# Kernel tuning notes

Measured on AMD Instinct MI355X. Metric: run time of the kernel, lower is better.

The kernel has to match this reference:

```python
import jax, jax.numpy as jnp
import numpy as np

NUM_CATEGORIES = 16
INPUT_DIM = 1024
HIDDEN_DIM = 4096
BATCH = 64
SEQ = 256


def setup_inputs() -> dict:
    key = jax.random.key(0)
    k1, k2, k3 = jax.random.split(key, 3)
    x = jax.random.normal(k1, (BATCH, SEQ, INPUT_DIM), dtype=jnp.float32)
    cat_ids = jax.random.randint(k2, (BATCH,), 0, NUM_CATEGORIES, dtype=jnp.int64)
    W = 0.02 * jax.random.normal(k3, (NUM_CATEGORIES, INPUT_DIM, HIDDEN_DIM), dtype=jnp.float32)
    b = jnp.zeros((NUM_CATEGORIES, HIDDEN_DIM), dtype=jnp.float32)
    return {"x": x, "cat_ids": cat_ids, "W": W, "b": b}


def reference(x, cat_ids, W, b):
    # Gather per-sample expert weights then batched matmul, matching torch.bmm semantics.
    selected_W = W[cat_ids]            # [B, input_dim, hidden_dim]
    selected_b = b[cat_ids]            # [B, hidden_dim]
    out = jnp.einsum('bsi,bih->bsh', x, selected_W) + selected_b[:, None, :]
    return out
```

## Files before the change

### kernel.cpp

```cpp
#include <hip/hip_runtime.h>
#include <hip/hip_bf16.h>
#include <stdint.h>

#define BATCH 64
#define SEQ   256
#define KDIM  1024
#define NDIM  4096
#define NCAT  16

#define BM 128
#define BN 128
#define BK 64
#define MT (SEQ/BM)
#define NT (NDIM/BN)
#define TILES_PER_BATCH (MT*NT)
#define NBLOCKS (BATCH*TILES_PER_BATCH)

typedef __attribute__((ext_vector_type(4))) float f32x4;
typedef __attribute__((ext_vector_type(4))) unsigned int u32x4;
typedef __attribute__((ext_vector_type(8))) short bf16x8;

__device__ __forceinline__ unsigned short f2bf(float f) {
  __hip_bfloat16 h = __float2bfloat16(f);
  return __builtin_bit_cast(unsigned short, h);
}
__device__ __forceinline__ unsigned pack2(float lo, float hi) {
  return (unsigned)f2bf(lo) | ((unsigned)f2bf(hi) << 16);
}
__device__ __forceinline__ void gload16(const void* g, void* l) {
  __builtin_amdgcn_global_load_lds(
      (const __attribute__((address_space(1))) unsigned int*)g,
      (__attribute__((address_space(3))) unsigned int*)l, 16, 0, 0);
}


#define CVT_W_BLOCKS (NCAT*(KDIM/64)*(NDIM/64))
#define CVT_X_BLOCKS ((BATCH*SEQ*KDIM/8)/256)

__global__ void cvt_fused(const float* __restrict__ x,
                          const float* __restrict__ W,
                          unsigned char* __restrict__ xb_t,
                          unsigned char* __restrict__ Wt) {
  __shared__ float ls[64][65];
  const int tid = threadIdx.x;

  if (blockIdx.x < CVT_W_BLOCKS) {
    const int bid = blockIdx.x;
    const int cat = bid >> 10;
    const int rem = bid & 1023;
    const int kt  = rem >> 6;
    const int ntl = rem & 63;

    const float* src = W + (size_t)cat * KDIM * NDIM + (size_t)(kt * 64) * NDIM + ntl * 64;
    const int kl = tid >> 4;
    const int nl = (tid & 15) * 4;
#pragma unroll
    for (int i = 0; i < 4; ++i) {
      f32x4 v = *(const f32x4*)(src + (size_t)(kl + i * 16) * NDIM + nl);
      ls[kl + i * 16][nl + 0] = v[0];
      ls[kl + i * 16][nl + 1] = v[1];
      ls[kl + i * 16][nl + 2] = v[2];
      ls[kl + i * 16][nl + 3] = v[3];
    }
    __syncthreads();
    const int n  = tid >> 2;
    const int k2 = (tid & 3) * 16;
    u32x4 q0, q1;
#pragma unroll
    for (int j = 0; j < 4; ++j) q0[j] = pack2(ls[k2 + 2 * j][n],     ls[k2 + 2 * j + 1][n]);
#pragma unroll
    for (int j = 0; j < 4; ++j) q1[j] = pack2(ls[k2 + 8 + 2 * j][n], ls[k2 + 9 + 2 * j][n]);

    const int nt   = ntl >> 2;
    const int sub  = ntl & 3;
    const int h    = sub >> 1;
    const int r    = (sub & 1) * 64 + n;
    const unsigned sw = ((unsigned)r & 7u) << 4;
    unsigned base = (unsigned)(cat * 8388608) + (unsigned)(nt * 524288)
                  + (unsigned)((kt * 2 + h) * 16384) + (unsigned)(r * 128);
    *(u32x4*)(Wt + base + (((unsigned)(k2 * 2))      ^ sw)) = q0;
    *(u32x4*)(Wt + base + (((unsigned)(k2 * 2 + 16)) ^ sw)) = q1;
  } else {
    int g = (blockIdx.x - CVT_W_BLOCKS) * 256 + tid;
    const int row = g >> 7;
    const int c   = g & 127;
    const int b   = row >> 8;
    const int s   = row & 255;
    const int kt  = c >> 3;
    const int ck  = c & 7;
    const int h   = s >> 7;
    const int r   = s & 127;
    const float* src = x + (size_t)row * KDIM + c * 8;
    f32x4 a = *(const f32x4*)src;
    f32x4 d = *(const f32x4*)(src + 4);
    u32x4 q;
    q[0] = pack2(a[0], a[1]); q[1] = pack2(a[2], a[3]);
    q[2] = pack2(d[0], d[1]); q[3] = pack2(d[2], d[3]);
    unsigned off = (unsigned)(((b * 16 + kt) * 2 + h) * 16384)
                 + (unsigned)(r * 128) + (((unsigned)(ck * 16)) ^ (((unsigned)r & 7u) << 4));
    *(u32x4*)(xb_t + off) = q;
  }
}

__global__ __launch_bounds__(256, 2)
void csl_gemm(const unsigned char* __restrict__ xb_t,
              const unsigned char* __restrict__ Wt,
              const int*   __restrict__ cat_ids,
              const float* __restrict__ bias,
              float* __restrict__ out)
{
  __shared__ __align__(16) unsigned char sA[BM * BK * 2];
  __shared__ __align__(16) unsigned char sB[BN * BK * 2];
  __shared__ int s_cat[BATCH];

  const int tid  = threadIdx.x;
  const int lane = tid & 63;
  const int wid  = tid >> 6;

  if (tid < BATCH) s_cat[tid] = cat_ids[tid];
  __syncthreads();

  const int bid  = (int)blockIdx.x;
  const int t_id = (NBLOCKS - 1) - ((bid & 7) * (NBLOCKS / 8) + (bid >> 3));

  const int myc = s_cat[lane];
  int c = 0, base = 0, cc = 0;
  unsigned long long mask = 0ULL;
  for (c = 0; c < NCAT; ++c) {
    mask = __ballot(myc == c);
    cc = __popcll(mask);
    int sz = cc * TILES_PER_BATCH;
    if (t_id < base + sz) break;
    base += sz;
  }
  if (c >= NCAT) return;
  const int idx    = t_id - base;
  const int per_nt = cc * MT;
  const int nt     = idx / per_nt;
  const int r      = idx % per_nt;
  const int want   = r >> 1;
  const int mt     = r & 1;
  unsigned long long mm = mask;
  for (int i = 0; i < want; ++i) mm &= (mm - 1);
  const int batch = __ffsll((long long)mm) - 1;
  const int cat   = c;

  const int m0 = mt * BM;
  const int n0 = nt * BN;

  const unsigned char* Ab = xb_t + (size_t)batch * 524288 + (unsigned)(mt * 16384);
  const unsigned char* Bb = Wt + (size_t)cat * 8388608 + (size_t)(nt >> 1) * 524288
                          + (unsigned)((nt & 1) * 16384);

  const unsigned tb16 = (unsigned)(tid * 16);

  const int lc        = lane & 15;
  const unsigned sw   = ((unsigned)lc & 7u) << 4;
  const unsigned kq16 = (unsigned)((lane >> 4) * 16);
  const unsigned koff0 = kq16 ^ sw;
  const unsigned koff1 = (64u + kq16) ^ sw;

  f32x4 acc[4][4] = {};
  const int wr = (wid >> 1) * 64;
  const int wc = (wid & 1) * 64;
  const unsigned rowA = (unsigned)((wr + lc) * 128);
  const unsigned rowB = (unsigned)((wc + lc) * 128);

  for (int kt = 0; kt < KDIM / BK; ++kt) {
    const unsigned ko = (unsigned)(kt * 32768);
    __syncthreads();
#pragma unroll
    for (int s = 0; s < 4; ++s)
      gload16(Ab + ko + (unsigned)(s * 4096) + tb16, sA + s * 4096 + tb16);
#pragma unroll
    for (int s = 0; s < 4; ++s)
      gload16(Bb + ko + (unsigned)(s * 4096) + tb16, sB + s * 4096 + tb16);
    __syncthreads();
#pragma unroll
    for (int kk = 0; kk < 2; ++kk) {
      const unsigned koff = kk ? koff1 : koff0;
      bf16x8 af[4], bfr[4];
#pragma unroll
      for (int mi = 0; mi < 4; ++mi)
        af[mi] = *(const bf16x8*)(sA + rowA + (unsigned)(mi * 2048) + koff);
#pragma unroll
      for (int ni = 0; ni < 4; ++ni)
        bfr[ni] = *(const bf16x8*)(sB + rowB + (unsigned)(ni * 2048) + koff);
#pragma unroll
      for (int mi = 0; mi < 4; ++mi)
#pragma unroll
        for (int ni = 0; ni < 4; ++ni)
          acc[mi][ni] = __builtin_amdgcn_mfma_f32_16x16x32_bf16(af[mi], bfr[ni], acc[mi][ni], 0, 0, 0);
    }
  }

  const int col_l = lane & 15;
  const int row_l = (lane >> 4) * 4;
  float bv4[4];
#pragma unroll
  for (int ni = 0; ni < 4; ++ni)
    bv4[ni] = bias[(size_t)cat * NDIM + (n0 + wc + ni * 16 + col_l)];
#pragma unroll
  for (int mi = 0; mi < 4; ++mi) {
#pragma unroll
    for (int ni = 0; ni < 4; ++ni) {
      int gr = m0 + wr + mi * 16 + row_l;
      int gc = n0 + wc + ni * 16 + col_l;
      f32x4 v = acc[mi][ni];
      size_t o = ((size_t)batch * SEQ + gr) * NDIM + gc;
      out[o]            = v[0] + bv4[ni];
      out[o + NDIM]     = v[1] + bv4[ni];
      out[o + 2 * NDIM] = v[2] + bv4[ni];
      out[o + 3 * NDIM] = v[3] + bv4[ni];
    }
  }
}

typedef __attribute__((ext_vector_type(2))) unsigned int u32x2;

__global__ __launch_bounds__(256, 2)
void csl_fallback(const float* __restrict__ x,
                  const int*   __restrict__ cat_ids,
                  const float* __restrict__ W,
                  const float* __restrict__ bias,
                  float* __restrict__ out)
{
  __shared__ __align__(16) unsigned char sA[BM * BK * 2];
  __shared__ __align__(16) unsigned char sB[BN * BK * 2];
  __shared__ int s_cat[BATCH];

  const int tid  = threadIdx.x;
  const int lane = tid & 63;
  const int wid  = tid >> 6;

  if (tid < BATCH) s_cat[tid] = cat_ids[tid];
  __syncthreads();

  const int myc = s_cat[lane];
  int t_id = (int)blockIdx.x;
  int c = 0, base = 0, cc = 0;
  unsigned long long mask = 0ULL;
  for (c = 0; c < NCAT; ++c) {
    mask = __ballot(myc == c);
    cc = __popcll(mask);
    int sz = cc * TILES_PER_BATCH;
    if (t_id < base + sz) break;
    base += sz;
  }
  if (c >= NCAT) return;
  const int idx    = t_id - base;
  const int per_nt = cc * MT;
  const int nt     = idx / per_nt;
  const int r      = idx % per_nt;
  const int want   = r >> 1;
  const int mt     = r & 1;
  unsigned long long mm = mask;
  for (int i = 0; i < want; ++i) mm &= (mm - 1);
  const int batch = __ffsll((long long)mm) - 1;
  const int cat   = c;

  const int m0 = mt * BM;
  const int n0 = nt * BN;

  const size_t x_base = ((size_t)batch * SEQ + m0) * KDIM;
  const size_t w_base = (size_t)cat * KDIM * NDIM + n0;

  f32x4 acc[4][4] = {};
  const int wr = (wid >> 1) * 64;
  const int wc = (wid & 1) * 64;

  for (int kt = 0; kt < KDIM / BK; ++kt) {
    const int k0 = kt * BK;
    f32x4 av[4][2];
#pragma unroll
    for (int s = 0; s < 4; ++s) {
      int seg  = tid + s * 256;
      int arow = seg >> 3;
      int ak   = (seg & 7) << 3;
      const float* gp = x + x_base + (size_t)arow * KDIM + (size_t)(k0 + ak);
      av[s][0] = *(const f32x4*)gp;
      av[s][1] = *(const f32x4*)(gp + 4);
    }
    f32x4 bv[2][4];
#pragma unroll
    for (int s = 0; s < 2; ++s) {
      int u  = tid + s * 256;
      int nq = u & 31;
      int kq = u >> 5;
      const float* gp = W + w_base + (size_t)(k0 + kq * 4) * NDIM + (size_t)(nq * 4);
#pragma unroll
      for (int rr = 0; rr < 4; ++rr)
        bv[s][rr] = *(const f32x4*)(gp + (size_t)rr * NDIM);
    }
    __syncthreads();
#pragma unroll
    for (int s = 0; s < 4; ++s) {
      int seg  = tid + s * 256;
      int arow = seg >> 3;
      int akb  = (seg & 7) << 4;
      unsigned byte = (unsigned)(arow * (BK * 2)) + ((unsigned)akb ^ (((unsigned)arow & 7u) << 4));
      u32x4 q;
      q[0] = pack2(av[s][0][0], av[s][0][1]);
      q[1] = pack2(av[s][0][2], av[s][0][3]);
      q[2] = pack2(av[s][1][0], av[s][1][1]);
      q[3] = pack2(av[s][1][2], av[s][1][3]);
      *(u32x4*)(sA + byte) = q;
    }
#pragma unroll
    for (int s = 0; s < 2; ++s) {
      int u  = tid + s * 256;
      int nq = u & 31;
      int kq = u >> 5;
      unsigned swz = ((unsigned)nq & 7u) << 4;
#pragma unroll
      for (int i = 0; i < 4; ++i) {
        int n = nq * 4 + i;
        unsigned byte = (unsigned)(n * (BK * 2)) + (((unsigned)(kq * 8)) ^ swz);
        u32x2 d;
        d[0] = pack2(bv[s][0][i], bv[s][1][i]);
        d[1] = pack2(bv[s][2][i], bv[s][3][i]);
        *(u32x2*)(sB + byte) = d;
      }
    }
    __syncthreads();
#pragma unroll
    for (int kk = 0; kk < 2; ++kk) {
      const int kb = kk * 64 + ((lane >> 4) << 4);
      bf16x8 af[4], bfr[4];
#pragma unroll
      for (int mi = 0; mi < 4; ++mi) {
        int row = wr + mi * 16 + (lane & 15);
        unsigned byte = (unsigned)(row * (BK * 2)) + ((unsigned)kb ^ (((unsigned)row & 7u) << 4));
        af[mi] = *(const bf16x8*)(sA + byte);
      }
#pragma unroll
      for (int ni = 0; ni < 4; ++ni) {
        int n = wc + ni * 16 + (lane & 15);
        unsigned byte = (unsigned)(n * (BK * 2)) + ((unsigned)kb ^ ((((unsigned)n >> 2) & 7u) << 4));
        bfr[ni] = *(const bf16x8*)(sB + byte);
      }
#pragma unroll
      for (int mi = 0; mi < 4; ++mi)
#pragma unroll
        for (int ni = 0; ni < 4; ++ni)
          acc[mi][ni] = __builtin_amdgcn_mfma_f32_16x16x32_bf16(af[mi], bfr[ni], acc[mi][ni], 0, 0, 0);
    }
  }

  const int col_l = lane & 15;
  const int row_l = (lane >> 4) * 4;
#pragma unroll
  for (int mi = 0; mi < 4; ++mi) {
#pragma unroll
    for (int ni = 0; ni < 4; ++ni) {
      int gr = m0 + wr + mi * 16 + row_l;
      int gc = n0 + wc + ni * 16 + col_l;
      float bvl = bias[(size_t)cat * NDIM + gc];
      f32x4 v = acc[mi][ni];
      size_t o = ((size_t)batch * SEQ + gr) * NDIM + gc;
      out[o]            = v[0] + bvl;
      out[o + NDIM]     = v[1] + bvl;
      out[o + 2 * NDIM] = v[2] + bvl;
      out[o + 3 * NDIM] = v[3] + bvl;
    }
  }
}

extern "C" void kernel_launch(void* const* d_in, const int* in_sizes, int n_in,
                              void* d_out, int out_size, void* d_ws, size_t ws_size,
                              hipStream_t stream) {
  const float* x       = (const float*)d_in[0];
  const int*   cat_ids = (const int*)d_in[1];
  const float* W       = (const float*)d_in[2];
  const float* bias    = (const float*)d_in[3];
  float*       out     = (float*)d_out;
  (void)in_sizes; (void)n_in; (void)out_size;

  const size_t wt_bytes = (size_t)NCAT * NDIM * KDIM * 2;
  const size_t xb_bytes = (size_t)BATCH * SEQ * KDIM * 2;
  const size_t need = wt_bytes + xb_bytes;

  if (ws_size >= need) {
    unsigned char* Wt   = (unsigned char*)d_ws;
    unsigned char* xb_t = Wt + wt_bytes;
    hipLaunchKernelGGL(cvt_fused, dim3(CVT_W_BLOCKS + CVT_X_BLOCKS), dim3(256), 0, stream,
                       x, W, xb_t, Wt);
    hipLaunchKernelGGL(csl_gemm, dim3(NBLOCKS), dim3(256), 0, stream,
                       xb_t, Wt, cat_ids, bias, out);
  } else {
    hipLaunchKernelGGL(csl_fallback, dim3(NBLOCKS), dim3(256), 0, stream,
                       x, cat_ids, W, bias, out);
  }
}
```

Baseline: 285.2 us.

## Enlarge GEMM tile to 256x128 covering full sequence per block

The grouped GEMM kernel now uses a 256x128 output tile, so each block covers the whole sequence for one batch and one N slice. Each wave computes a 128x64 sub-tile with 32 MFMA accumulators instead of 16, and the grid halves. This is meant to reuse each loaded W tile across twice as many rows, cutting LDS and global traffic per FLOP. The tile-order mapping also changes to drop the reversed ordering. In exchange, register pressure and LDS use go up, which may lower occupancy under launch_bounds(256,2), and fewer blocks may hurt load balance.

```diff
diff --git a/kernel.cpp b/kernel.cpp
--- a/kernel.cpp
+++ b/kernel.cpp
@@ -15,6 +15,11 @@
 #define NT (NDIM/BN)
 #define TILES_PER_BATCH (MT*NT)
 #define NBLOCKS (BATCH*TILES_PER_BATCH)
+
+#define GBM 256
+#define GBN 128
+#define G_NT (NDIM/GBN)
+#define G_NBLOCKS (BATCH*G_NT)
 
 typedef __attribute__((ext_vector_type(4))) float f32x4;
 typedef __attribute__((ext_vector_type(4))) unsigned int u32x4;
@@ -109,6 +114,123 @@
               const float* __restrict__ bias,
               float* __restrict__ out)
 {
+  __shared__ __align__(16) unsigned char sA[GBM * BK * 2];
+  __shared__ __align__(16) unsigned char sB[GBN * BK * 2];
+  __shared__ int s_cat[BATCH];
+
+  const int tid  = threadIdx.x;
+  const int lane = tid & 63;
+  const int wid  = tid >> 6;
+  const int wm   = wid >> 1;
+  const int wn   = wid & 1;
+
+  if (tid < BATCH) s_cat[tid] = cat_ids[tid];
+  __syncthreads();
+
+  const int bid  = (int)blockIdx.x;
+  const int t_id = (bid & 7) * (G_NBLOCKS / 8) + (bid >> 3);
+
+  const int myc = s_cat[lane];
+  int c = 0, base = 0, cc = 0;
+  unsigned long long mask = 0ULL;
+  for (c = 0; c < NCAT; ++c) {
+    mask = __ballot(myc == c);
+    cc = __popcll(mask);
+    int sz = cc * G_NT;
+    if (t_id < base + sz) break;
+    base += sz;
+  }
+  if (c >= NCAT) return;
+  const int idx = t_id - base;
+  const int nt  = idx / cc;
+  const int pos = idx % cc;
+  unsigned long long mm = mask;
+  for (int i = 0; i < pos; ++i) mm &= (mm - 1);
+  const int batch = __ffsll((long long)mm) - 1;
+  const int cat   = c;
+
+  const int n0 = nt * GBN;
+
+  const unsigned char* Ab = xb_t + (size_t)batch * 524288;
+  const unsigned char* Bb = Wt + (size_t)cat * 8388608 + (size_t)(nt >> 1) * 524288
+                          + (unsigned)((nt & 1) * 16384);
+
+  const unsigned tb16 = (unsigned)(tid * 16);
+
+  const int lc        = lane & 15;
+  const unsigned sw   = ((unsigned)lc & 7u) << 4;
+  const unsigned kq16 = (unsigned)((lane >> 4) * 16);
+  const unsigned koff0 = kq16 ^ sw;
+  const unsigned koff1 = (64u + kq16) ^ sw;
+
+  f32x4 acc[8][4] = {};
+  const unsigned rA   = (unsigned)(wm * 16384 + lc * 128);
+  const unsigned rowB = (unsigned)(wn * 8192 + lc * 128);
+
+  for (int kt = 0; kt < KDIM / BK; ++kt) {
+    const unsigned ko = (unsigned)(kt * 32768);
+    __syncthreads();
+#pragma unroll
+    for (int s = 0; s < 8; ++s)
+      gload16(Ab + ko + (unsigned)(s * 4096) + tb16, sA + s * 4096 + tb16);
+#pragma unroll
+    for (int s = 0; s < 4; ++s)
+      gload16(Bb + ko + (unsigned)(s * 4096) + tb16, sB + s * 4096 + tb16);
+    __syncthreads();
+#pragma unroll
+    for (int kk = 0; kk < 2; ++kk) {
+      const unsigned koff = kk ? koff1 : koff0;
+      bf16x8 bfr[4];
+#pragma unroll
+      for (int ni = 0; ni < 4; ++ni)
+        bfr[ni] = *(const bf16x8*)(sB + rowB + (unsigned)(ni * 2048) + koff);
+#pragma unroll
+      for (int mh = 0; mh < 2; ++mh) {
+        bf16x8 af[4];
+#pragma unroll
+        for (int mi = 0; mi < 4; ++mi)
+          af[mi] = *(const bf16x8*)(sA + rA + (unsigned)(mh * 8192 + mi * 2048) + koff);
+#pragma unroll
+        for (int mi = 0; mi < 4; ++mi)
+#pragma unroll
+          for (int ni = 0; ni < 4; ++ni)
+            acc[mh * 4 + mi][ni] = __builtin_amdgcn_mfma_f32_16x16x32_bf16(
+                af[mi], bfr[ni], acc[mh * 4 + mi][ni], 0, 0, 0);
+      }
+    }
+  }
+
+  const int col_l = lane & 15;
+  const int row_l = (lane >> 4) * 4;
+  float bv4[4];
+#pragma unroll
+  for (int ni = 0; ni < 4; ++ni)
+    bv4[ni] = bias[(size_t)cat * NDIM + (n0 + wn * 64 + ni * 16 + col_l)];
+#pragma unroll
+  for (int mf = 0; mf < 8; ++mf) {
+#pragma unroll
+    for (int ni = 0; ni < 4; ++ni) {
+      int gr = wm * 128 + (mf >> 2) * 64 + (mf & 3) * 16 + row_l;
+      int gc = n0 + wn * 64 + ni * 16 + col_l;
+      f32x4 v = acc[mf][ni];
+      size_t o = ((size_t)batch * SEQ + gr) * NDIM + gc;
+      out[o]            = v[0] + bv4[ni];
+      out[o + NDIM]     = v[1] + bv4[ni];
+      out[o + 2 * NDIM] = v[2] + bv4[ni];
+      out[o + 3 * NDIM] = v[3] + bv4[ni];
+    }
+  }
+}
+
+typedef __attribute__((ext_vector_type(2))) unsigned int u32x2;
+
+__global__ __launch_bounds__(256, 2)
+void csl_fallback(const float* __restrict__ x,
+                  const int*   __restrict__ cat_ids,
+                  const float* __restrict__ W,
+                  const float* __restrict__ bias,
+                  float* __restrict__ out)
+{
   __shared__ __align__(16) unsigned char sA[BM * BK * 2];
   __shared__ __align__(16) unsigned char sB[BN * BK * 2];
   __shared__ int s_cat[BATCH];
@@ -120,10 +242,8 @@
   if (tid < BATCH) s_cat[tid] = cat_ids[tid];
   __syncthreads();
 
-  const int bid  = (int)blockIdx.x;
-  const int t_id = (NBLOCKS - 1) - ((bid & 7) * (NBLOCKS / 8) + (bid >> 3));
-
   const int myc = s_cat[lane];
+  int t_id = (int)blockIdx.x;
   int c = 0, base = 0, cc = 0;
   unsigned long long mask = 0ULL;
   for (c = 0; c < NCAT; ++c) {
@@ -148,120 +268,6 @@
   const int m0 = mt * BM;
   const int n0 = nt * BN;
 
-  const unsigned char* Ab = xb_t + (size_t)batch * 524288 + (unsigned)(mt * 16384);
-  const unsigned char* Bb = Wt + (size_t)cat * 8388608 + (size_t)(nt >> 1) * 524288
-                          + (unsigned)((nt & 1) * 16384);
-
-  const unsigned tb16 = (unsigned)(tid * 16);
-
-  const int lc        = lane & 15;
-  const unsigned sw   = ((unsigned)lc & 7u) << 4;
-  const unsigned kq16 = (unsigned)((lane >> 4) * 16);
-  const unsigned koff0 = kq16 ^ sw;
-  const unsigned koff1 = (64u + kq16) ^ sw;
-
-  f32x4 acc[4][4] = {};
-  const int wr = (wid >> 1) * 64;
-  const int wc = (wid & 1) * 64;
-  const unsigned rowA = (unsigned)((wr + lc) * 128);
-  const unsigned rowB = (unsigned)((wc + lc) * 128);
-
-  for (int kt = 0; kt < KDIM / BK; ++kt) {
-    const unsigned ko = (unsigned)(kt * 32768);
-    __syncthreads();
-#pragma unroll
-    for (int s = 0; s < 4; ++s)
-      gload16(Ab + ko + (unsigned)(s * 4096) + tb16, sA + s * 4096 + tb16);
-#pragma unroll
-    for (int s = 0; s < 4; ++s)
-      gload16(Bb + ko + (unsigned)(s * 4096) + tb16, sB + s * 4096 + tb16);
-    __syncthreads();
-#pragma unroll
-    for (int kk = 0; kk < 2; ++kk) {
-      const unsigned koff = kk ? koff1 : koff0;
-      bf16x8 af[4], bfr[4];
-#pragma unroll
-      for (int mi = 0; mi < 4; ++mi)
-        af[mi] = *(const bf16x8*)(sA + rowA + (unsigned)(mi * 2048) + koff);
-#pragma unroll
-      for (int ni = 0; ni < 4; ++ni)
-        bfr[ni] = *(const bf16x8*)(sB + rowB + (unsigned)(ni * 2048) + koff);
-#pragma unroll
-      for (int mi = 0; mi < 4; ++mi)
-#pragma unroll
-        for (int ni = 0; ni < 4; ++ni)
-          acc[mi][ni] = __builtin_amdgcn_mfma_f32_16x16x32_bf16(af[mi], bfr[ni], acc[mi][ni], 0, 0, 0);
-    }
-  }
-
-  const int col_l = lane & 15;
-  const int row_l = (lane >> 4) * 4;
-  float bv4[4];
-#pragma unroll
-  for (int ni = 0; ni < 4; ++ni)
-    bv4[ni] = bias[(size_t)cat * NDIM + (n0 + wc + ni * 16 + col_l)];
-#pragma unroll
-  for (int mi = 0; mi < 4; ++mi) {
-#pragma unroll
-    for (int ni = 0; ni < 4; ++ni) {
-      int gr = m0 + wr + mi * 16 + row_l;
-      int gc = n0 + wc + ni * 16 + col_l;
-      f32x4 v = acc[mi][ni];
-      size_t o = ((size_t)batch * SEQ + gr) * NDIM + gc;
-      out[o]            = v[0] + bv4[ni];
-      out[o + NDIM]     = v[1] + bv4[ni];
-      out[o + 2 * NDIM] = v[2] + bv4[ni];
-      out[o + 3 * NDIM] = v[3] + bv4[ni];
-    }
-  }
-}
-
-typedef __attribute__((ext_vector_type(2))) unsigned int u32x2;
-
-__global__ __launch_bounds__(256, 2)
-void csl_fallback(const float* __restrict__ x,
-                  const int*   __restrict__ cat_ids,
-                  const float* __restrict__ W,
-                  const float* __restrict__ bias,
-                  float* __restrict__ out)
-{
-  __shared__ __align__(16) unsigned char sA[BM * BK * 2];
-  __shared__ __align__(16) unsigned char sB[BN * BK * 2];
-  __shared__ int s_cat[BATCH];
-
-  const int tid  = threadIdx.x;
-  const int lane = tid & 63;
-  const int wid  = tid >> 6;
-
-  if (tid < BATCH) s_cat[tid] = cat_ids[tid];
-  __syncthreads();
-
-  const int myc = s_cat[lane];
-  int t_id = (int)blockIdx.x;
-  int c = 0, base = 0, cc = 0;
-  unsigned long long mask = 0ULL;
-  for (c = 0; c < NCAT; ++c) {
-    mask = __ballot(myc == c);
-    cc = __popcll(mask);
-    int sz = cc * TILES_PER_BATCH;
-    if (t_id < base + sz) break;
-    base += sz;
-  }
-  if (c >= NCAT) return;
-  const int idx    = t_id - base;
-  const int per_nt = cc * MT;
-  const int nt     = idx / per_nt;
-  const int r      = idx % per_nt;
-  const int want   = r >> 1;
-  const int mt     = r & 1;
-  unsigned long long mm = mask;
-  for (int i = 0; i < want; ++i) mm &= (mm - 1);
-  const int batch = __ffsll((long long)mm) - 1;
-  const int cat   = c;
-
-  const int m0 = mt * BM;
-  const int n0 = nt * BN;
-
   const size_t x_base = ((size_t)batch * SEQ + m0) * KDIM;
   const size_t w_base = (size_t)cat * KDIM * NDIM + n0;
 
@@ -385,7 +391,7 @@
     unsigned char* xb_t = Wt + wt_bytes;
     hipLaunchKernelGGL(cvt_fused, dim3(CVT_W_BLOCKS + CVT_X_BLOCKS), dim3(256), 0, stream,
                        x, W, xb_t, Wt);
-    hipLaunchKernelGGL(csl_gemm, dim3(NBLOCKS), dim3(256), 0, stream,
+    hipLaunchKernelGGL(csl_gemm, dim3(G_NBLOCKS), dim3(256), 0, stream,
                        xb_t, Wt, cat_ids, bias, out);
   } else {
     hipLaunchKernelGGL(csl_fallback, dim3(NBLOCKS), dim3(256), 0, stream,
```

After: 259.0 us, median of 3. 9.2% less time.
